# Performance work log

Measured on AMD Instinct MI355X. Metric: run time of the kernel, lower is better.

The kernel has to match this reference:

```python
import jax, jax.numpy as jnp
import numpy as np

B, S, H, D = 8, 1024, 16, 64
W = H * D  # hidden width = 1024


def setup_inputs() -> dict:
    key = jax.random.key(0)
    ks = jax.random.split(key, 5)
    std = 0.02
    return {
        "from_tensor": jax.random.normal(ks[0], (B, S, W), dtype=jnp.float32),
        "to_tensor": jax.random.normal(ks[1], (B, S, W), dtype=jnp.float32),
        "Wq": jax.random.normal(ks[2], (W, W), dtype=jnp.float32) * std,
        "bq": jnp.zeros((W,), dtype=jnp.float32),
        "Wk": jax.random.normal(ks[3], (W, W), dtype=jnp.float32) * std,
        "bk": jnp.zeros((W,), dtype=jnp.float32),
        "Wv": jax.random.normal(ks[4], (W, W), dtype=jnp.float32) * std,
        "bv": jnp.zeros((W,), dtype=jnp.float32),
    }


def reference(from_tensor, to_tensor, Wq, bq, Wk, bk, Wv, bv):
    # Q/K/V projections (no activations: query_act=key_act=value_act=None)
    q = from_tensor @ Wq + bq  # [B, S, W]
    k = to_tensor @ Wk + bk
    v = to_tensor @ Wv + bv
    # split heads -> [B, H, S, D]
    q = q.reshape(B, S, H, D).transpose(0, 2, 1, 3)
    k = k.reshape(B, S, H, D).transpose(0, 2, 1, 3)
    v = v.reshape(B, S, H, D).transpose(0, 2, 1, 3)
    scale = 1.0 / np.sqrt(float(D))
    scores = jnp.einsum("bhqd,bhkd->bhqk", q, k) * scale  # [B, H, S, S]
    # attention_mask=None, dropout_prob=0.0 -> no mask, no dropout
    probs = jax.nn.softmax(scores, axis=-1)
    ctx = jnp.einsum("bhqk,bhkd->bhqd", probs, v)  # [B, H, S, D]
    # merge heads -> [B, S, H*D] (do_return_2d_tensor=False)
    return ctx.transpose(0, 2, 1, 3).reshape(B, S, H * D)
```

## Files before the change

kernel.cpp:

```cpp
#include <hip/hip_runtime.h>
#include <hip/hip_bf16.h>
#include <math.h>


#define B_ 8
#define S_ 1024
#define H_ 16
#define D_ 64
#define W_ 1024

typedef __bf16 bf16x8 __attribute__((ext_vector_type(8)));
typedef float f32x4 __attribute__((ext_vector_type(4)));
typedef unsigned short ushort_t;

#define MFMA16(a, b, c) __builtin_amdgcn_mfma_f32_16x16x32_bf16((a), (b), (c), 0, 0, 0)

__device__ inline ushort_t f2bf(float f) {
    unsigned int u = __float_as_uint(f);
    u += 0x7fff + ((u >> 16) & 1);
    return (ushort_t)(u >> 16);
}

__device__ inline ushort_t f2bf_rhu(float f) {
    return (ushort_t)((__float_as_uint(f) + 0x8000u) >> 16);
}

__device__ inline void async16(const void* g, void* l) {
    __builtin_amdgcn_global_load_lds((const __attribute__((address_space(1))) void*)g,
                                     (__attribute__((address_space(3))) void*)l, 16, 0, 0);
}

__global__ __launch_bounds__(256) void cast2_bf16(const float* __restrict__ a,
                                                  const float* __restrict__ b,
                                                  ushort_t* __restrict__ da,
                                                  ushort_t* __restrict__ db, int n4) {
    int i = blockIdx.x * 256 + threadIdx.x;
    if (i >= n4) return;
    const float* src = blockIdx.y ? b : a;
    ushort_t* dst = blockIdx.y ? db : da;
    float4 v = ((const float4*)src)[i];
    ushort4 o;
    o.x = f2bf(v.x); o.y = f2bf(v.y); o.z = f2bf(v.z); o.w = f2bf(v.w);
    ((ushort4*)dst)[i] = o;
}

__global__ __launch_bounds__(256) void transpose_cast(const float* __restrict__ Wq,
                                                      const float* __restrict__ Wk,
                                                      const float* __restrict__ Wv,
                                                      ushort_t* __restrict__ Wt) {
    __shared__ float tile[32][33];
    int z = blockIdx.z;
    const float* src = (z == 0) ? Wq : (z == 1 ? Wk : Wv);
    ushort_t* dst = Wt + (size_t)z * W_ * W_;
    int tx = threadIdx.x, ty = threadIdx.y;
    int x = blockIdx.x * 32 + tx;
#pragma unroll
    for (int jj = 0; jj < 4; jj++) {
        int y = blockIdx.y * 32 + ty + jj * 8;
        tile[ty + jj * 8][tx] = src[(size_t)y * W_ + x];
    }
    __syncthreads();
    int x2 = blockIdx.y * 32 + tx;
#pragma unroll
    for (int jj = 0; jj < 4; jj++) {
        int y2 = blockIdx.x * 32 + ty + jj * 8;
        dst[(size_t)y2 * W_ + x2] = f2bf(tile[tx][ty + jj * 8]);
    }
}

__global__ __launch_bounds__(256) void qkv_gemm(const ushort_t* __restrict__ fromB,
                                                const ushort_t* __restrict__ toB,
                                                const ushort_t* __restrict__ Wt,
                                                const float* __restrict__ bq,
                                                const float* __restrict__ bk,
                                                const float* __restrict__ bv,
                                                ushort_t* __restrict__ Qd,
                                                ushort_t* __restrict__ Kd,
                                                ushort_t* __restrict__ Vt) {
    __shared__ __attribute__((aligned(16))) ushort_t As[128 * 32];
    __shared__ __attribute__((aligned(16))) ushort_t Bs[128 * 32];
    int z = blockIdx.y;
    const ushort_t* A = (z == 0) ? fromB : toB;
    const ushort_t* Bt = Wt + (size_t)z * (W_ * W_);
    const float* bias = (z == 0) ? bq : (z == 1 ? bk : bv);
    ushort_t* dst = (z == 0) ? Qd : (z == 1 ? Kd : Vt);

    int bx = blockIdx.x;
    int j64 = bx >> 3;
    int mTile = ((bx & 7) << 3) | (j64 >> 3);
    int nTile = j64 & 7;
    int mBase = mTile * 128, nBase = nTile * 128;

    int t = threadIdx.x;
    int lane = t & 63, w = t >> 6;
    int wm = w >> 1, wn = w & 1;
    int ln = lane & 15, qd = lane >> 4;
    int wb = t & ~63;

    f32x4 zero = {0.f, 0.f, 0.f, 0.f};
    f32x4 acc[4][4];
#pragma unroll
    for (int i = 0; i < 4; i++)
#pragma unroll
        for (int j = 0; j < 4; j++) acc[i][j] = zero;

    for (int kt = 0; kt < 32; ++kt) {
        int k0 = kt * 32;
#pragma unroll
        for (int c = 0; c < 2; ++c) {
            int idx16 = c * 256 + t;
            int row = idx16 >> 2, seg = idx16 & 3;
            async16(A + (size_t)(mBase + row) * W_ + k0 + seg * 8, As + (size_t)(c * 256 + wb) * 8);
            async16(Bt + (size_t)(nBase + row) * W_ + k0 + seg * 8, Bs + (size_t)(c * 256 + wb) * 8);
        }
        __syncthreads();
        bf16x8 af[4], bfr[4];
#pragma unroll
        for (int i = 0; i < 4; i++) af[i] = *(const bf16x8*)(As + (wm * 64 + i * 16 + ln) * 32 + qd * 8);
#pragma unroll
        for (int j = 0; j < 4; j++) bfr[j] = *(const bf16x8*)(Bs + (wn * 64 + j * 16 + ln) * 32 + qd * 8);
#pragma unroll
        for (int i = 0; i < 4; i++)
#pragma unroll
            for (int j = 0; j < 4; j++) acc[i][j] = MFMA16(af[i], bfr[j], acc[i][j]);
        __syncthreads();
    }

#pragma unroll
    for (int j = 0; j < 4; j++) {
        int n = nBase + wn * 64 + j * 16 + ln;
        float bb = bias[n];
        int h = n >> 6, d = n & 63;
#pragma unroll
        for (int i = 0; i < 4; i++) {
            int mrow = mBase + wm * 64 + i * 16 + qd * 4;
#pragma unroll
            for (int r = 0; r < 4; r++) {
                int m = mrow + r;
                int b = m >> 10, s = m & 1023;
                float v = acc[i][j][r] + bb;
                if (z == 0) v *= 0.18033688011111773f;
                size_t idx;
                if (z < 2) idx = ((size_t)(b * H_ + h) * S_ + s) * D_ + d;
                else       idx = ((size_t)(b * H_ + h) * D_ + d) * S_ + s;
                dst[idx] = f2bf(v);
            }
        }
    }
}

__global__ __launch_bounds__(256, 3) void attn(const ushort_t* __restrict__ Qd,
                                               const ushort_t* __restrict__ Kd,
                                               const ushort_t* __restrict__ Vt,
                                               float* __restrict__ out) {
    __shared__ __attribute__((aligned(16))) ushort_t Ks[2][4096];
    __shared__ __attribute__((aligned(16))) ushort_t Vs[2][4096];
    __shared__ __attribute__((aligned(16))) ushort_t Plds[4][32][72];

    int bh = blockIdx.y;
    int t = threadIdx.x, w = t >> 6, lane = t & 63;
    int ln = lane & 15, qd = lane >> 4;
    int qbase = blockIdx.x * 128 + w * 32;
    const ushort_t* Qb = Qd + (size_t)bh * S_ * D_;
    const ushort_t* Kb = Kd + (size_t)bh * S_ * D_;
    const ushort_t* Vb = Vt + (size_t)bh * D_ * S_;

    bf16x8 qf[2][2];
#pragma unroll
    for (int i = 0; i < 2; i++) {
        const ushort_t* qp = Qb + (size_t)(qbase + i * 16 + ln) * D_ + qd * 8;
        qf[i][0] = *(const bf16x8*)qp;
        qf[i][1] = *(const bf16x8*)(qp + 32);
    }

    int l8 = lane >> 3, s8 = lane & 7;
    int stgOff = (s8 ^ l8) << 3;
    const ushort_t* kg = Kb + (size_t)(w * 16 + l8) * D_ + stgOff;
    const ushort_t* vg = Vb + (size_t)(w * 16 + l8) * S_ + stgOff;
    int kOff = ln * 64 + ((qd ^ (ln & 7)) << 3);

    float rs[2][4];
    f32x4 zero = {0.f, 0.f, 0.f, 0.f};
    f32x4 accO[2][4];
#pragma unroll
    for (int i = 0; i < 2; i++) {
        rs[i][0] = rs[i][1] = rs[i][2] = rs[i][3] = 0.f;
#pragma unroll
        for (int jd = 0; jd < 4; jd++) accO[i][jd] = zero;
    }

    async16(kg, &Ks[0][w * 1024]);
    async16(kg + 8 * D_, &Ks[0][w * 1024 + 512]);
    async16(vg, &Vs[0][w * 1024]);
    async16(vg + 8 * S_, &Vs[0][w * 1024 + 512]);

    for (int c = 0; c < 16; ++c) {
        int buf = c & 1;
        __builtin_amdgcn_s_waitcnt(0x0F70);
        __syncthreads();
        if (c + 1 < 16) {
            int kc = (c + 1) * 64;
            async16(kg + (size_t)kc * D_, &Ks[buf ^ 1][w * 1024]);
            async16(kg + (size_t)kc * D_ + 8 * D_, &Ks[buf ^ 1][w * 1024 + 512]);
            async16(vg + kc, &Vs[buf ^ 1][w * 1024]);
            async16(vg + kc + 8 * S_, &Vs[buf ^ 1][w * 1024 + 512]);
        }

        f32x4 sc[2][4];
#pragma unroll
        for (int i = 0; i < 2; i++)
#pragma unroll
            for (int j = 0; j < 4; j++) sc[i][j] = zero;
        __builtin_amdgcn_s_setprio(1);
#pragma unroll
        for (int j = 0; j < 4; j++) {
            bf16x8 k0 = *(const bf16x8*)&Ks[buf][j * 1024 + kOff];
            bf16x8 k1 = *(const bf16x8*)&Ks[buf][(j * 1024 + kOff) ^ 32];
#pragma unroll
            for (int i = 0; i < 2; i++) {
                sc[i][j] = MFMA16(qf[i][0], k0, sc[i][j]);
                sc[i][j] = MFMA16(qf[i][1], k1, sc[i][j]);
            }
        }
        __builtin_amdgcn_s_setprio(0);
#pragma unroll
        for (int i = 0; i < 2; i++)
#pragma unroll
            for (int j = 0; j < 4; j++)
#pragma unroll
                for (int r = 0; r < 4; r++) {
                    float p = exp2f(sc[i][j][r]);
                    rs[i][r] += p;
                    Plds[w][i * 16 + qd * 4 + r][j * 16 + ln] = f2bf_rhu(p);
                }
        bf16x8 pf[2][2];
#pragma unroll
        for (int i = 0; i < 2; i++) {
            pf[i][0] = *(const bf16x8*)&Plds[w][i * 16 + ln][qd * 8];
            pf[i][1] = *(const bf16x8*)&Plds[w][i * 16 + ln][32 + qd * 8];
        }
        __builtin_amdgcn_s_setprio(1);
#pragma unroll
        for (int jd = 0; jd < 4; jd++) {
            bf16x8 v0 = *(const bf16x8*)&Vs[buf][jd * 1024 + kOff];
            bf16x8 v1 = *(const bf16x8*)&Vs[buf][(jd * 1024 + kOff) ^ 32];
#pragma unroll
            for (int i = 0; i < 2; i++) {
                accO[i][jd] = MFMA16(pf[i][0], v0, accO[i][jd]);
                accO[i][jd] = MFMA16(pf[i][1], v1, accO[i][jd]);
            }
        }
        __builtin_amdgcn_s_setprio(0);
    }

    int b = bh >> 4, h = bh & 15;
#pragma unroll
    for (int i = 0; i < 2; i++)
#pragma unroll
        for (int r = 0; r < 4; r++) {
            float s = rs[i][r];
            s += __shfl_xor(s, 1);
            s += __shfl_xor(s, 2);
            s += __shfl_xor(s, 4);
            s += __shfl_xor(s, 8);
            float inv = 1.f / s;
            int q = qbase + i * 16 + qd * 4 + r;
            float* op = out + ((size_t)(b * S_ + q) * H_ + h) * D_;
#pragma unroll
            for (int jd = 0; jd < 4; jd++) op[jd * 16 + ln] = accO[i][jd][r] * inv;
        }
}

extern "C" void kernel_launch(void* const* d_in, const int* in_sizes, int n_in,
                              void* d_out, int out_size, void* d_ws, size_t ws_size,
                              hipStream_t stream) {
    const float* from = (const float*)d_in[0];
    const float* to_  = (const float*)d_in[1];
    const float* Wq = (const float*)d_in[2];
    const float* bq = (const float*)d_in[3];
    const float* Wk = (const float*)d_in[4];
    const float* bk = (const float*)d_in[5];
    const float* Wv = (const float*)d_in[6];
    const float* bv = (const float*)d_in[7];
    float* out = (float*)d_out;

    const size_t NTOK = (size_t)B_ * S_ * W_;
    ushort_t* ws = (ushort_t*)d_ws;
    ushort_t* fromB = ws;
    ushort_t* toB = fromB + NTOK;
    ushort_t* Wt = toB + NTOK;
    ushort_t* Qd = Wt + (size_t)3 * W_ * W_;
    ushort_t* Kd = Qd + NTOK;
    ushort_t* Vt = Kd + NTOK;

    int n4 = (int)(NTOK / 4);
    cast2_bf16<<<dim3(n4 / 256, 2), dim3(256), 0, stream>>>(from, to_, fromB, toB, n4);
    transpose_cast<<<dim3(32, 32, 3), dim3(32, 8), 0, stream>>>(Wq, Wk, Wv, Wt);
    qkv_gemm<<<dim3(512, 3), dim3(256), 0, stream>>>(fromB, toB, Wt, bq, bk, bv, Qd, Kd, Vt);
    attn<<<dim3(8, 128), dim3(256), 0, stream>>>(Qd, Kd, Vt, out);
}
```

Measured before the change: 276.1 us.

## Rewrite QKV GEMM as 256x256 tile, 8-wave, double-buffered pipelined kernel

Replaces the 128x128 single-buffered QKV projection GEMM with a 256x256-tile, 512-thread kernel. It double-buffers K=64 slices in LDS with asynchronous global-to-LDS loads, interleaves prefetch with MFMA issue using raw barriers and vmcnt waits, and XOR-swizzles LDS to avoid bank conflicts. The three projections are merged into one 1D grid with an XCD-aware tile mapping. The goal is to hide global load latency and raise MFMA utilization, at the cost of more LDS and register pressure plus fragile hand-written synchronization.

```diff
diff --git a/kernel.cpp b/kernel.cpp
--- a/kernel.cpp
+++ b/kernel.cpp
@@ -29,6 +29,9 @@
     __builtin_amdgcn_global_load_lds((const __attribute__((address_space(1))) void*)g,
                                      (__attribute__((address_space(3))) void*)l, 16, 0, 0);
 }
+
+#define RAW_BARRIER() asm volatile("s_barrier" ::: "memory")
+#define VMCNT(n) asm volatile("s_waitcnt vmcnt(" #n ")" ::: "memory")
 
 __global__ __launch_bounds__(256) void cast2_bf16(const float* __restrict__ a,
                                                   const float* __restrict__ b,
@@ -68,78 +71,142 @@
     }
 }
 
-__global__ __launch_bounds__(256) void qkv_gemm(const ushort_t* __restrict__ fromB,
-                                                const ushort_t* __restrict__ toB,
-                                                const ushort_t* __restrict__ Wt,
-                                                const float* __restrict__ bq,
-                                                const float* __restrict__ bk,
-                                                const float* __restrict__ bv,
-                                                ushort_t* __restrict__ Qd,
-                                                ushort_t* __restrict__ Kd,
-                                                ushort_t* __restrict__ Vt) {
-    __shared__ __attribute__((aligned(16))) ushort_t As[128 * 32];
-    __shared__ __attribute__((aligned(16))) ushort_t Bs[128 * 32];
-    int z = blockIdx.y;
+__global__ __launch_bounds__(512, 2) void qkv_gemm8(const ushort_t* __restrict__ fromB,
+                                                    const ushort_t* __restrict__ toB,
+                                                    const ushort_t* __restrict__ Wt,
+                                                    const float* __restrict__ bq,
+                                                    const float* __restrict__ bk,
+                                                    const float* __restrict__ bv,
+                                                    ushort_t* __restrict__ Qd,
+                                                    ushort_t* __restrict__ Kd,
+                                                    ushort_t* __restrict__ Vt) {
+    __shared__ __attribute__((aligned(16))) ushort_t As[2 * 2 * 8192];
+    __shared__ __attribute__((aligned(16))) ushort_t Bs[2 * 2 * 8192];
+
+    int bid = blockIdx.x;
+    int xcd = bid & 7, jb = bid >> 3;
+    int mTile = xcd * 4 + (jb & 3);
+    int nTile = jb >> 2;
+    int mBase = mTile << 8, nBase = nTile << 8;
+    int z = nTile >> 2;
     const ushort_t* A = (z == 0) ? fromB : toB;
-    const ushort_t* Bt = Wt + (size_t)z * (W_ * W_);
     const float* bias = (z == 0) ? bq : (z == 1 ? bk : bv);
     ushort_t* dst = (z == 0) ? Qd : (z == 1 ? Kd : Vt);
-
-    int bx = blockIdx.x;
-    int j64 = bx >> 3;
-    int mTile = ((bx & 7) << 3) | (j64 >> 3);
-    int nTile = j64 & 7;
-    int mBase = mTile * 128, nBase = nTile * 128;
+    float qscale = (z == 0) ? 0.18033688011111773f : 1.0f;
 
     int t = threadIdx.x;
     int lane = t & 63, w = t >> 6;
-    int wm = w >> 1, wn = w & 1;
+    int wm = w >> 2, wn = w & 3;
     int ln = lane & 15, qd = lane >> 4;
     int wb = t & ~63;
+    int fs = (qd ^ ((ln >> 1) & 3)) << 3;
+
+    int rowL0 = t >> 2;
+    int sG = ((t & 3) ^ ((t >> 3) & 3)) << 3;
+    const ushort_t* pA0 = A + (size_t)(mBase + rowL0) * W_ + sG;
+    const ushort_t* pA1 = A + (size_t)(mBase + 128 + rowL0) * W_ + sG;
+    const ushort_t* pB0 = Wt + (size_t)(nBase + rowL0) * W_ + sG;
+    const ushort_t* pB1 = Wt + (size_t)(nBase + 128 + rowL0) * W_ + sG;
+    int d0 = wb * 8;
+    int d1 = (512 + wb) * 8;
 
     f32x4 zero = {0.f, 0.f, 0.f, 0.f};
-    f32x4 acc[4][4];
-#pragma unroll
-    for (int i = 0; i < 4; i++)
-#pragma unroll
-        for (int j = 0; j < 4; j++) acc[i][j] = zero;
-
-    for (int kt = 0; kt < 32; ++kt) {
-        int k0 = kt * 32;
-#pragma unroll
-        for (int c = 0; c < 2; ++c) {
-            int idx16 = c * 256 + t;
-            int row = idx16 >> 2, seg = idx16 & 3;
-            async16(A + (size_t)(mBase + row) * W_ + k0 + seg * 8, As + (size_t)(c * 256 + wb) * 8);
-            async16(Bt + (size_t)(nBase + row) * W_ + k0 + seg * 8, Bs + (size_t)(c * 256 + wb) * 8);
-        }
-        __syncthreads();
-        bf16x8 af[4], bfr[4];
-#pragma unroll
-        for (int i = 0; i < 4; i++) af[i] = *(const bf16x8*)(As + (wm * 64 + i * 16 + ln) * 32 + qd * 8);
-#pragma unroll
-        for (int j = 0; j < 4; j++) bfr[j] = *(const bf16x8*)(Bs + (wn * 64 + j * 16 + ln) * 32 + qd * 8);
-#pragma unroll
-        for (int i = 0; i < 4; i++)
-#pragma unroll
-            for (int j = 0; j < 4; j++) acc[i][j] = MFMA16(af[i], bfr[j], acc[i][j]);
-        __syncthreads();
-    }
-
-#pragma unroll
-    for (int j = 0; j < 4; j++) {
-        int n = nBase + wn * 64 + j * 16 + ln;
-        float bb = bias[n];
-        int h = n >> 6, d = n & 63;
-#pragma unroll
-        for (int i = 0; i < 4; i++) {
-            int mrow = mBase + wm * 64 + i * 16 + qd * 4;
+    f32x4 acc[8][4];
+#pragma unroll
+    for (int i = 0; i < 8; i++)
+#pragma unroll
+        for (int jj = 0; jj < 4; jj++) acc[i][jj] = zero;
+
+    async16(pA0, As + d0); async16(pA1, As + d1);
+    async16(pB0, Bs + d0); async16(pB1, Bs + d1);
+    async16(pA0 + 32, As + 8192 + d0); async16(pA1 + 32, As + 8192 + d1);
+    async16(pB0 + 32, Bs + 8192 + d0); async16(pB1 + 32, Bs + 8192 + d1);
+
+    int aw = wm * 128 + ln;
+    int bw = wn * 64 + ln;
+
+    for (int kt = 0; kt < 16; ++kt) {
+        int buf = kt & 1, nb = buf ^ 1;
+        int hb0 = (buf << 14);
+        int hb1 = hb0 + 8192;
+        int nh0 = (nb << 14);
+        int nh1 = nh0 + 8192;
+        int nOff = (kt + 1) << 6;
+        bool pf = kt < 15;
+
+        bf16x8 af[8], b0, b1, b2, b3;
+
+        VMCNT(4);
+        RAW_BARRIER();
+        if (pf) { async16(pA0 + nOff, As + nh0 + d0); async16(pA1 + nOff, As + nh0 + d1); }
+#pragma unroll
+        for (int i = 0; i < 8; i++) af[i] = *(const bf16x8*)(As + hb0 + (aw + i * 16) * 32 + fs);
+        b0 = *(const bf16x8*)(Bs + hb0 + bw * 32 + fs);
+        b1 = *(const bf16x8*)(Bs + hb0 + (bw + 16) * 32 + fs);
+        __builtin_amdgcn_s_setprio(1);
+#pragma unroll
+        for (int i = 0; i < 8; i++) {
+            acc[i][0] = MFMA16(af[i], b0, acc[i][0]);
+            acc[i][1] = MFMA16(af[i], b1, acc[i][1]);
+        }
+        __builtin_amdgcn_s_setprio(0);
+        RAW_BARRIER();
+
+        if (pf) { async16(pB0 + nOff, Bs + nh0 + d0); async16(pB1 + nOff, Bs + nh0 + d1); }
+        b2 = *(const bf16x8*)(Bs + hb0 + (bw + 32) * 32 + fs);
+        b3 = *(const bf16x8*)(Bs + hb0 + (bw + 48) * 32 + fs);
+        __builtin_amdgcn_s_setprio(1);
+#pragma unroll
+        for (int i = 0; i < 8; i++) {
+            acc[i][2] = MFMA16(af[i], b2, acc[i][2]);
+            acc[i][3] = MFMA16(af[i], b3, acc[i][3]);
+        }
+        __builtin_amdgcn_s_setprio(0);
+        RAW_BARRIER();
+
+        if (pf) { VMCNT(4); } else { VMCNT(0); }
+        RAW_BARRIER();
+        if (pf) { async16(pA0 + nOff + 32, As + nh1 + d0); async16(pA1 + nOff + 32, As + nh1 + d1); }
+#pragma unroll
+        for (int i = 0; i < 8; i++) af[i] = *(const bf16x8*)(As + hb1 + (aw + i * 16) * 32 + fs);
+        b0 = *(const bf16x8*)(Bs + hb1 + bw * 32 + fs);
+        b1 = *(const bf16x8*)(Bs + hb1 + (bw + 16) * 32 + fs);
+        __builtin_amdgcn_s_setprio(1);
+#pragma unroll
+        for (int i = 0; i < 8; i++) {
+            acc[i][0] = MFMA16(af[i], b0, acc[i][0]);
+            acc[i][1] = MFMA16(af[i], b1, acc[i][1]);
+        }
+        __builtin_amdgcn_s_setprio(0);
+        RAW_BARRIER();
+
+        if (pf) { async16(pB0 + nOff + 32, Bs + nh1 + d0); async16(pB1 + nOff + 32, Bs + nh1 + d1); }
+        b2 = *(const bf16x8*)(Bs + hb1 + (bw + 32) * 32 + fs);
+        b3 = *(const bf16x8*)(Bs + hb1 + (bw + 48) * 32 + fs);
+        __builtin_amdgcn_s_setprio(1);
+#pragma unroll
+        for (int i = 0; i < 8; i++) {
+            acc[i][2] = MFMA16(af[i], b2, acc[i][2]);
+            acc[i][3] = MFMA16(af[i], b3, acc[i][3]);
+        }
+        __builtin_amdgcn_s_setprio(0);
+        RAW_BARRIER();
+    }
+
+#pragma unroll
+    for (int jj = 0; jj < 4; jj++) {
+        int n = nBase + wn * 64 + jj * 16 + ln;
+        int nn = n & 1023;
+        float bb = bias[nn];
+        int h = nn >> 6, d = nn & 63;
+#pragma unroll
+        for (int i = 0; i < 8; i++) {
+            int mrow = mBase + wm * 128 + i * 16 + qd * 4;
 #pragma unroll
             for (int r = 0; r < 4; r++) {
                 int m = mrow + r;
                 int b = m >> 10, s = m & 1023;
-                float v = acc[i][j][r] + bb;
-                if (z == 0) v *= 0.18033688011111773f;
+                float v = (acc[i][jj][r] + bb) * qscale;
                 size_t idx;
                 if (z < 2) idx = ((size_t)(b * H_ + h) * S_ + s) * D_ + d;
                 else       idx = ((size_t)(b * H_ + h) * D_ + d) * S_ + s;
@@ -296,6 +363,6 @@
     int n4 = (int)(NTOK / 4);
     cast2_bf16<<<dim3(n4 / 256, 2), dim3(256), 0, stream>>>(from, to_, fromB, toB, n4);
     transpose_cast<<<dim3(32, 32, 3), dim3(32, 8), 0, stream>>>(Wq, Wk, Wv, Wt);
-    qkv_gemm<<<dim3(512, 3), dim3(256), 0, stream>>>(fromB, toB, Wt, bq, bk, bv, Qd, Kd, Vt);
+    qkv_gemm8<<<dim3(384), dim3(512), 0, stream>>>(fromB, toB, Wt, bq, bk, bv, Qd, Kd, Vt);
     attn<<<dim3(8, 128), dim3(256), 0, stream>>>(Qd, Kd, Vt, out);
 }
```

Result: slower. 309.0 us (+11.9%).
